# Optimization experiments

Measured on AMD Instinct MI355X. Metric: run time of the kernel, lower is better.

Reference implementation:

```python
import jax, jax.numpy as jnp
import numpy as np

B, S, H = 2, 1024, 2880
I = 2880
E = 16
K = 4


def setup_inputs() -> dict:
    key = jax.random.key(0)
    ks = jax.random.split(key, 4)
    sc = 0.02  # init scale to keep activations in a sane range
    return {
        "x": jax.random.normal(ks[0], (B, S, H), jnp.float32),
        "gate_w": jax.random.normal(ks[1], (E, H), jnp.float32) * sc,
        "gate_b": jnp.zeros((E,), jnp.float32),
        "w_gate_up": jax.random.normal(ks[2], (E, 2 * I, H), jnp.float32) * sc,
        "b_gate_up": jnp.zeros((E, 2 * I), jnp.float32),
        "w_down": jax.random.normal(ks[3], (E, H, I), jnp.float32) * sc,
        "b_down": jnp.zeros((E, H), jnp.float32),
        "swiglu_alpha": jnp.full((E,), 1.702, jnp.float32),
        "swiglu_beta": jnp.full((E,), 1.0, jnp.float32),
        "swiglu_limit": jnp.full((E,), 7.0, jnp.float32),
    }


def reference(x, gate_w, gate_b, w_gate_up, b_gate_up, w_down, b_down,
              swiglu_alpha, swiglu_beta, swiglu_limit):
    orig_shape = x.shape
    hidden = orig_shape[-1]
    t = x.reshape(-1, hidden)  # [T, H]
    T = t.shape[0]

    # Router: gate linear -> top-k -> renormalize via softmax over selected logits
    logits = t @ gate_w.T + gate_b  # [T, E]
    top_vals, top_idx = jax.lax.top_k(logits, K)  # [T, K]
    top_w = jax.nn.softmax(top_vals, axis=-1)  # RenormalizeMoeRoutingMethod
    # Dense combine matrix [T, E]; zero for non-selected experts
    combine = jnp.zeros((T, E), t.dtype).at[jnp.arange(T)[:, None], top_idx].set(top_w)

    def expert_body(acc, params):
        wgu, bgu, wd, bd, alpha, beta, lim, cw = params
        h = t @ wgu.T + bgu  # [T, 2I] fused gate_up
        glu, lin = jnp.split(h, 2, axis=-1)  # FUSED_GATE_UP_PROJ chunk
        glu = jnp.minimum(glu, lim)  # swiglu_limit clamp (gpt-oss)
        lin = jnp.clip(lin, -lim, lim)
        act = glu * jax.nn.sigmoid(alpha * glu) * (lin + beta)  # [T, I]
        y = act @ wd.T + bd  # [T, H]
        return acc + cw[:, None] * y, None

    init = jnp.zeros((T, hidden), t.dtype)
    out, _ = jax.lax.scan(
        expert_body, init,
        (w_gate_up, b_gate_up, w_down, b_down,
         swiglu_alpha, swiglu_beta, swiglu_limit, combine.T))
    return out.reshape(orig_shape)
```

## Files before the change

### kernel.cpp

```cpp
#include <hip/hip_runtime.h>
#include <stdint.h>
#include <math.h>

#define T_TOK 2048
#define H_DIM 2880
#define I_DIM 2880
#define E_NUM 16
#define TOPK 4

#define BT 128
#define BK 64
#define NK 45
#define MT_MAX 16
#define NT1 45
#define NT2 45

typedef __bf16 bf16_t;
typedef __bf16 bf16x8 __attribute__((ext_vector_type(8)));
typedef __bf16 bf16x4 __attribute__((ext_vector_type(4)));
typedef float f32x4 __attribute__((ext_vector_type(4)));

#define WAITV(N) asm volatile("s_waitcnt vmcnt(" #N ")" ::: "memory")
#define WAITL()  asm volatile("s_waitcnt lgkmcnt(0)" ::: "memory")
#define BAR()    asm volatile("s_barrier" ::: "memory")

__device__ __forceinline__ void gload16(const bf16_t* g, bf16_t* l) {
  __builtin_amdgcn_global_load_lds(
      (__attribute__((address_space(1))) const uint32_t*)g,
      (__attribute__((address_space(3))) uint32_t*)l, 16, 0, 0);
}

__device__ __forceinline__ f32x4 mfma16(bf16x8 a, bf16x8 b, f32x4 c) {
  return __builtin_amdgcn_mfma_f32_16x16x32_bf16(a, b, c, 0, 0, 0);
}

__global__ void k_prep(const float* __restrict__ x, bf16_t* __restrict__ xbf,
                       int* __restrict__ counts) {
  if (blockIdx.x == 0 && threadIdx.x < E_NUM) counts[threadIdx.x] = 0;
  int idx = blockIdx.x * 256 + threadIdx.x;
  const int total = T_TOK * H_DIM / 8;
  if (idx < total) {
    f32x4 a = ((const f32x4*)x)[2 * idx];
    f32x4 b = ((const f32x4*)x)[2 * idx + 1];
    bf16x8 o = {(bf16_t)a[0], (bf16_t)a[1], (bf16_t)a[2], (bf16_t)a[3],
                (bf16_t)b[0], (bf16_t)b[1], (bf16_t)b[2], (bf16_t)b[3]};
    ((bf16x8*)xbf)[idx] = o;
  }
}

__global__ void k_router(const float* __restrict__ x, const float* __restrict__ gw,
                         const float* __restrict__ gb, float* __restrict__ topw,
                         int* __restrict__ counts, int* __restrict__ rowsl) {
  const int t = blockIdx.x;
  const int lane = threadIdx.x;
  const int c = lane >> 4, e = lane & 15;
  const f32x4* x4 = (const f32x4*)(x + (size_t)t * H_DIM);
  const f32x4* w4 = (const f32x4*)(gw + (size_t)e * H_DIM);
  float p = 0.f;
  const int per = (H_DIM / 4) / 4;
  for (int i = c * per; i < (c + 1) * per; ++i) {
    f32x4 xv = x4[i], wv = w4[i];
    p += xv[0] * wv[0] + xv[1] * wv[1] + xv[2] * wv[2] + xv[3] * wv[3];
  }
  p += __shfl_xor(p, 16);
  p += __shfl_xor(p, 32);
  p += gb[e];
  __shared__ float lg[E_NUM];
  if (lane < E_NUM) lg[lane] = p;
  __syncthreads();
  if (lane == 0) {
    float v[E_NUM];
    #pragma unroll
    for (int i = 0; i < E_NUM; ++i) v[i] = lg[i];
    int idxs[TOPK]; float vals[TOPK];
    for (int k = 0; k < TOPK; ++k) {
      int bi = 0; float bv = -1e30f;
      for (int i = 0; i < E_NUM; ++i) {
        if (v[i] > bv) { bv = v[i]; bi = i; }
      }
      idxs[k] = bi; vals[k] = bv; v[bi] = -1e30f;
    }
    float m = vals[0], s = 0.f, w[TOPK];
    for (int k = 0; k < TOPK; ++k) { w[k] = expf(vals[k] - m); s += w[k]; }
    for (int k = 0; k < TOPK; ++k) {
      int slot = t * TOPK + k;
      topw[slot] = w[k] / s;
      int pos = atomicAdd(&counts[idxs[k]], 1);
      rowsl[idxs[k] * T_TOK + pos] = slot;
    }
  }
}


#define G1_STAGE_T(KT, BUF) do {                                        \
    int c1_ = (KT) > (NK - 1) ? (NK - 1) : (KT);                        \
    _Pragma("unroll")                                                   \
    for (int i_ = 0; i_ < 4; ++i_)                                      \
      gload16(tsrc[i_] + c1_ * BK, &sT[BUF][w * 2048 + i_ * 512]);      \
  } while (0)

#define G1_MFMA(CUR) do {                                               \
    _Pragma("unroll")                                                   \
    for (int ks = 0; ks < 2; ++ks) {                                    \
      const int koff = ks * 32 + (lane >> 4) * 8;                       \
      bf16x8 wg_[2], wl_[2], tf[4];                                     \
      _Pragma("unroll")                                                 \
      for (int wi = 0; wi < 2; ++wi) {                                  \
        int rg = 32 * wm + 16 * wi + (lane & 15);                       \
        int swz = koff ^ ((rg & 7) << 3);                               \
        wg_[wi] = *(const bf16x8*)(&sW[CUR][rg * 64 + swz]);            \
        wl_[wi] = *(const bf16x8*)(&sW[CUR][(rg + 64) * 64 + swz]);     \
      }                                                                 \
      _Pragma("unroll")                                                 \
      for (int tj = 0; tj < 4; ++tj) {                                  \
        int rt = 64 * wt + 16 * tj + (lane & 15);                       \
        tf[tj] = *(const bf16x8*)(&sT[CUR][rt * 64 + (koff ^ ((rt & 7) << 3))]); \
      }                                                                 \
      _Pragma("unroll")                                                 \
      for (int wi = 0; wi < 2; ++wi)                                    \
        _Pragma("unroll")                                               \
        for (int tj = 0; tj < 4; ++tj) {                                \
          accg[wi][tj] = mfma16(wg_[wi], tf[tj], accg[wi][tj]);         \
          accl[wi][tj] = mfma16(wl_[wi], tf[tj], accl[wi][tj]);         \
        }                                                               \
    }                                                                   \
  } while (0)

#define G1_ITER(KK, WSET) do {                                          \
    const int cur_ = (KK) & 1;                                          \
    G1_STAGE_T((KK) + 1, cur_ ^ 1);                                     \
    _Pragma("unroll")                                                   \
    for (int p_ = 0; p_ < 8; ++p_) {                                    \
      bf16x4 b_ = {(bf16_t)WSET[p_][0], (bf16_t)WSET[p_][1],            \
                   (bf16_t)WSET[p_][2], (bf16_t)WSET[p_][3]};           \
      *(bf16x4*)(&sW[cur_ ^ 1][wo[p_]]) = b_;                           \
    }                                                                   \
    { int c3_ = (KK) + 3 > (NK - 1) ? (NK - 1) : (KK) + 3;              \
      _Pragma("unroll")                                                 \
      for (int p_ = 0; p_ < 8; ++p_)                                    \
        WSET[p_] = *(const f32x4*)(wbase + wgo[p_] + c3_ * BK); }       \
    __builtin_amdgcn_s_setprio(1);                                      \
    G1_MFMA(cur_);                                                      \
    __builtin_amdgcn_s_setprio(0);                                      \
    WAITV(8); WAITL(); BAR();                                           \
  } while (0)

__global__ __launch_bounds__(256, 2)
void k_gemm1(const bf16_t* __restrict__ xbf, const float* __restrict__ wgu,
             const float* __restrict__ bgu, const float* __restrict__ al,
             const float* __restrict__ be, const float* __restrict__ lim_,
             const int* __restrict__ counts, const int* __restrict__ rowsl,
             bf16_t* __restrict__ act) {
  const int nwg = E_NUM * NT1 * MT_MAX;
  const int L = (blockIdx.x & 7) * (nwg >> 3) + (blockIdx.x >> 3);
  const int mt = L & (MT_MAX - 1);
  const int t2 = L >> 4;
  const int nt = t2 % NT1;
  const int e  = t2 / NT1;
  const int Ne = counts[e];
  const int m0 = mt * BT;
  if (m0 >= Ne) return;
  const int n0 = nt * 64;

  __shared__ alignas(16) bf16_t sW[2][128 * 64];
  __shared__ alignas(16) bf16_t sT[2][128 * 64];

  const int tid = threadIdx.x;
  const int w = tid >> 6, lane = tid & 63;
  const int wm = w & 1, wt = w >> 1;
  const int* rl = rowsl + e * T_TOK;

  const bf16_t* tsrc[4];
  {
    const int r_ = lane >> 3, cc = lane & 7;
    #pragma unroll
    for (int i = 0; i < 4; ++i) {
      int r = w * 32 + i * 8 + r_;
      int li = m0 + r; if (li > Ne - 1) li = Ne - 1;
      int tok = rl[li] >> 2;
      tsrc[i] = xbf + (size_t)tok * H_DIM + ((cc ^ (r & 7)) << 3);
    }
  }

  const int wrow = tid >> 4, wf = tid & 15;
  const float* wbase = wgu + (size_t)e * (2 * I_DIM) * H_DIM + wf * 4;
  int wgo[8], wo[8];
  #pragma unroll
  for (int p = 0; p < 8; ++p) {
    int row = wrow + p * 16;
    int grow = (row < 64) ? (n0 + row) : (I_DIM + n0 + row - 64);
    wgo[p] = grow * H_DIM;
    wo[p] = row * 64 + ((wf * 4) ^ ((row & 7) << 3));
  }

  f32x4 zero = {0.f, 0.f, 0.f, 0.f};
  f32x4 accg[2][4], accl[2][4];
  #pragma unroll
  for (int i = 0; i < 2; ++i)
    #pragma unroll
    for (int j = 0; j < 4; ++j) { accg[i][j] = zero; accl[i][j] = zero; }

  f32x4 wA[8], wB[8];
  #pragma unroll
  for (int p = 0; p < 8; ++p) wA[p] = *(const f32x4*)(wbase + wgo[p]);
  WAITV(0);
  #pragma unroll
  for (int p = 0; p < 8; ++p) {
    bf16x4 b = {(bf16_t)wA[p][0], (bf16_t)wA[p][1],
                (bf16_t)wA[p][2], (bf16_t)wA[p][3]};
    *(bf16x4*)(&sW[0][wo[p]]) = b;
  }
  G1_STAGE_T(0, 0);
  #pragma unroll
  for (int p = 0; p < 8; ++p) wA[p] = *(const f32x4*)(wbase + wgo[p] + 1 * BK);
  #pragma unroll
  for (int p = 0; p < 8; ++p) wB[p] = *(const f32x4*)(wbase + wgo[p] + 2 * BK);
  WAITV(8);
  WAITL(); BAR();

  for (int kb = 0; kb < NK - 1; kb += 2) {
    G1_ITER(kb, wA);
    G1_ITER(kb + 1, wB);
  }
  G1_ITER(NK - 1, wA);

  const float alpha = al[e], beta = be[e], lim = lim_[e];
  const float* bgp = bgu + (size_t)e * (2 * I_DIM);
  #pragma unroll
  for (int wi = 0; wi < 2; ++wi) {
    const int nb = n0 + 32 * wm + 16 * wi + ((lane >> 4) << 2);
    f32x4 bg4 = *(const f32x4*)(bgp + nb);
    f32x4 bl4 = *(const f32x4*)(bgp + I_DIM + nb);
    #pragma unroll
    for (int tj = 0; tj < 4; ++tj) {
      const int li2 = m0 + 64 * wt + 16 * tj + (lane & 15);
      if (li2 < Ne) {
        const int slot = rl[li2];
        bf16x4 ov;
        #pragma unroll
        for (int r = 0; r < 4; ++r) {
          float g = accg[wi][tj][r] + bg4[r];
          float l = accl[wi][tj][r] + bl4[r];
          g = fminf(g, lim);
          l = fminf(fmaxf(l, -lim), lim);
          float sg = 1.0f / (1.0f + expf(-alpha * g));
          ov[r] = (bf16_t)(g * sg * (l + beta));
        }
        *(bf16x4*)(&act[(size_t)slot * I_DIM + nb]) = ov;
      }
    }
  }
}


#define G2_STAGE_T(KT, BUF) do {                                        \
    int c1_ = (KT) > (NK - 1) ? (NK - 1) : (KT);                        \
    _Pragma("unroll")                                                   \
    for (int i_ = 0; i_ < 4; ++i_)                                      \
      gload16(tsrc[i_] + c1_ * BK, &sT[BUF][w * 2048 + i_ * 512]);      \
  } while (0)

#define G2_MFMA(CUR) do {                                               \
    _Pragma("unroll")                                                   \
    for (int ks = 0; ks < 2; ++ks) {                                    \
      const int koff = ks * 32 + (lane >> 4) * 8;                       \
      bf16x8 wf_[2], tf[4];                                             \
      _Pragma("unroll")                                                 \
      for (int wi = 0; wi < 2; ++wi) {                                  \
        int rg = 32 * wm + 16 * wi + (lane & 15);                       \
        wf_[wi] = *(const bf16x8*)(&sW[CUR][rg * 64 + (koff ^ ((rg & 7) << 3))]); \
      }                                                                 \
      _Pragma("unroll")                                                 \
      for (int tj = 0; tj < 4; ++tj) {                                  \
        int rt = 64 * wt + 16 * tj + (lane & 15);                       \
        tf[tj] = *(const bf16x8*)(&sT[CUR][rt * 64 + (koff ^ ((rt & 7) << 3))]); \
      }                                                                 \
      _Pragma("unroll")                                                 \
      for (int wi = 0; wi < 2; ++wi)                                    \
        _Pragma("unroll")                                               \
        for (int tj = 0; tj < 4; ++tj)                                  \
          acc[wi][tj] = mfma16(wf_[wi], tf[tj], acc[wi][tj]);           \
    }                                                                   \
  } while (0)

#define G2_ITER(KK, WSET) do {                                          \
    const int cur_ = (KK) & 1;                                          \
    G2_STAGE_T((KK) + 1, cur_ ^ 1);                                     \
    _Pragma("unroll")                                                   \
    for (int p_ = 0; p_ < 4; ++p_) {                                    \
      bf16x4 b_ = {(bf16_t)WSET[p_][0], (bf16_t)WSET[p_][1],            \
                   (bf16_t)WSET[p_][2], (bf16_t)WSET[p_][3]};           \
      *(bf16x4*)(&sW[cur_ ^ 1][wo[p_]]) = b_;                           \
    }                                                                   \
    { int c3_ = (KK) + 3 > (NK - 1) ? (NK - 1) : (KK) + 3;              \
      _Pragma("unroll")                                                 \
      for (int p_ = 0; p_ < 4; ++p_)                                    \
        WSET[p_] = *(const f32x4*)(wbase + wgo[p_] + c3_ * BK); }       \
    __builtin_amdgcn_s_setprio(1);                                      \
    G2_MFMA(cur_);                                                      \
    __builtin_amdgcn_s_setprio(0);                                      \
    WAITV(4); WAITL(); BAR();                                           \
  } while (0)

__global__ __launch_bounds__(256, 3)
void k_gemm2(const bf16_t* __restrict__ act, const float* __restrict__ wd,
             const float* __restrict__ bd, const float* __restrict__ topw,
             const int* __restrict__ counts, const int* __restrict__ rowsl,
             float* __restrict__ ybuf) {
  const int nwg = E_NUM * NT2 * MT_MAX;
  const int L = (blockIdx.x & 7) * (nwg >> 3) + (blockIdx.x >> 3);
  const int mt = L & (MT_MAX - 1);
  const int t2 = L >> 4;
  const int ht = t2 % NT2;
  const int e  = t2 / NT2;
  const int Ne = counts[e];
  const int m0 = mt * BT;
  if (m0 >= Ne) return;
  const int h0 = ht * 64;

  __shared__ alignas(16) bf16_t sW[2][64 * 64];
  __shared__ alignas(16) bf16_t sT[2][128 * 64];

  const int tid = threadIdx.x;
  const int w = tid >> 6, lane = tid & 63;
  const int wm = w & 1, wt = w >> 1;
  const int* rl = rowsl + e * T_TOK;

  const bf16_t* tsrc[4];
  {
    const int r_ = lane >> 3, cc = lane & 7;
    #pragma unroll
    for (int i = 0; i < 4; ++i) {
      int r = w * 32 + i * 8 + r_;
      int li = m0 + r; if (li > Ne - 1) li = Ne - 1;
      int slot = rl[li];
      tsrc[i] = act + (size_t)slot * I_DIM + ((cc ^ (r & 7)) << 3);
    }
  }

  const int wrow = tid >> 4, wf = tid & 15;
  const float* wbase = wd + (size_t)e * H_DIM * I_DIM + wf * 4;
  int wgo[4], wo[4];
  #pragma unroll
  for (int p = 0; p < 4; ++p) {
    int row = wrow + p * 16;
    wgo[p] = (h0 + row) * I_DIM;
    wo[p] = row * 64 + ((wf * 4) ^ ((row & 7) << 3));
  }

  f32x4 zero = {0.f, 0.f, 0.f, 0.f};
  f32x4 acc[2][4];
  #pragma unroll
  for (int i = 0; i < 2; ++i)
    #pragma unroll
    for (int j = 0; j < 4; ++j) acc[i][j] = zero;

  f32x4 wA[4], wB[4];
  #pragma unroll
  for (int p = 0; p < 4; ++p) wA[p] = *(const f32x4*)(wbase + wgo[p]);
  WAITV(0);
  #pragma unroll
  for (int p = 0; p < 4; ++p) {
    bf16x4 b = {(bf16_t)wA[p][0], (bf16_t)wA[p][1],
                (bf16_t)wA[p][2], (bf16_t)wA[p][3]};
    *(bf16x4*)(&sW[0][wo[p]]) = b;
  }
  G2_STAGE_T(0, 0);
  #pragma unroll
  for (int p = 0; p < 4; ++p) wA[p] = *(const f32x4*)(wbase + wgo[p] + 1 * BK);
  #pragma unroll
  for (int p = 0; p < 4; ++p) wB[p] = *(const f32x4*)(wbase + wgo[p] + 2 * BK);
  WAITV(4);
  WAITL(); BAR();

  for (int kb = 0; kb < NK - 1; kb += 2) {
    G2_ITER(kb, wA);
    G2_ITER(kb + 1, wB);
  }
  G2_ITER(NK - 1, wA);

  const float* bdp = bd + (size_t)e * H_DIM;
  #pragma unroll
  for (int wi = 0; wi < 2; ++wi) {
    const int hb = h0 + 32 * wm + 16 * wi + ((lane >> 4) << 2);
    f32x4 b4 = *(const f32x4*)(bdp + hb);
    #pragma unroll
    for (int tj = 0; tj < 4; ++tj) {
      const int li2 = m0 + 64 * wt + 16 * tj + (lane & 15);
      if (li2 < Ne) {
        const int slot = rl[li2];
        const float tw = topw[slot];
        f32x4 o = (acc[wi][tj] + b4) * tw;
        *(f32x4*)(&ybuf[(size_t)slot * H_DIM + hb]) = o;
      }
    }
  }
}

__global__ void k_combine(const float* __restrict__ ybuf, float* __restrict__ out) {
  const int j4 = H_DIM / 4;
  int idx = blockIdx.x * 256 + threadIdx.x;
  if (idx >= T_TOK * j4) return;
  int t = idx / j4, j = idx - t * j4;
  const f32x4* yb = (const f32x4*)ybuf;
  f32x4 s = yb[(size_t)(t * 4 + 0) * j4 + j];
  s = s + yb[(size_t)(t * 4 + 1) * j4 + j];
  s = s + yb[(size_t)(t * 4 + 2) * j4 + j];
  s = s + yb[(size_t)(t * 4 + 3) * j4 + j];
  ((f32x4*)out)[idx] = s;
}

extern "C" void kernel_launch(void* const* d_in, const int* in_sizes, int n_in,
                              void* d_out, int out_size, void* d_ws, size_t ws_size,
                              hipStream_t stream) {
  const float* x   = (const float*)d_in[0];
  const float* gw  = (const float*)d_in[1];
  const float* gb  = (const float*)d_in[2];
  const float* wgu = (const float*)d_in[3];
  const float* bgu = (const float*)d_in[4];
  const float* wd  = (const float*)d_in[5];
  const float* bd  = (const float*)d_in[6];
  const float* sal = (const float*)d_in[7];
  const float* sbe = (const float*)d_in[8];
  const float* sli = (const float*)d_in[9];
  float* out = (float*)d_out;

  char* ws = (char*)d_ws;
  int*    counts = (int*)(ws + 0);
  int*    rowsl  = (int*)(ws + 4096);
  float*  topw   = (float*)(ws + 4096 + 131072);
  bf16_t* xbf    = (bf16_t*)(ws + (1 << 20));
  bf16_t* act    = (bf16_t*)(ws + (size_t)(16 << 20));
  float*  ybuf   = (float*)(ws + (size_t)(64 << 20));

  k_prep<<<dim3(2880), dim3(256), 0, stream>>>(x, xbf, counts);
  k_router<<<dim3(T_TOK), dim3(64), 0, stream>>>(x, gw, gb, topw, counts, rowsl);
  k_gemm1<<<dim3(E_NUM * NT1 * MT_MAX), dim3(256), 0, stream>>>(
      xbf, wgu, bgu, sal, sbe, sli, counts, rowsl, act);
  k_gemm2<<<dim3(E_NUM * NT2 * MT_MAX), dim3(256), 0, stream>>>(
      act, wd, bd, topw, counts, rowsl, ybuf);
  k_combine<<<dim3(5760), dim3(256), 0, stream>>>(ybuf, out);
}
```

Before: 1.403 ms.

## Double token tile to 256 with 512-thread blocks in both expert GEMMs

Raises the token tile per workgroup from 128 to 256 and runs both expert GEMMs with 8 waves (512 threads) instead of 4. Each fp32 weight tile is then loaded and converted to bf16 once per 256 routed tokens rather than once per 128, halving repeated weight fetch and conversion work per expert. The per-thread weight staging share shrinks to match, and LDS for the token tile doubles. In exchange there are half as many workgroups, so partially filled tiles waste more work when an expert has few tokens, and register and LDS pressure per CU changes under the new launch bounds.

```diff
diff --git a/kernel.cpp b/kernel.cpp
--- a/kernel.cpp
+++ b/kernel.cpp
@@ -8,10 +8,10 @@
 #define E_NUM 16
 #define TOPK 4
 
-#define BT 128
+#define BT 256
 #define BK 64
 #define NK 45
-#define MT_MAX 16
+#define MT_MAX 8
 #define NT1 45
 #define NT2 45
 
@@ -92,11 +92,11 @@
 }
 
 
-#define G1_STAGE_T(KT, BUF) do {                                        \
+#define G_STAGE_T(KT, BUF) do {                                         \
     int c1_ = (KT) > (NK - 1) ? (NK - 1) : (KT);                        \
     _Pragma("unroll")                                                   \
     for (int i_ = 0; i_ < 4; ++i_)                                      \
-      gload16(tsrc[i_] + c1_ * BK, &sT[BUF][w * 2048 + i_ * 512]);      \
+      gload16(tsrc[i_] + c1_ * BK, &sT[BUF][wv * 2048 + i_ * 512]);     \
   } while (0)
 
 #define G1_MFMA(CUR) do {                                               \
@@ -128,24 +128,24 @@
 
 #define G1_ITER(KK, WSET) do {                                          \
     const int cur_ = (KK) & 1;                                          \
-    G1_STAGE_T((KK) + 1, cur_ ^ 1);                                     \
+    G_STAGE_T((KK) + 1, cur_ ^ 1);                                      \
     _Pragma("unroll")                                                   \
-    for (int p_ = 0; p_ < 8; ++p_) {                                    \
+    for (int p_ = 0; p_ < 4; ++p_) {                                    \
       bf16x4 b_ = {(bf16_t)WSET[p_][0], (bf16_t)WSET[p_][1],            \
                    (bf16_t)WSET[p_][2], (bf16_t)WSET[p_][3]};           \
       *(bf16x4*)(&sW[cur_ ^ 1][wo[p_]]) = b_;                           \
     }                                                                   \
     { int c3_ = (KK) + 3 > (NK - 1) ? (NK - 1) : (KK) + 3;              \
       _Pragma("unroll")                                                 \
-      for (int p_ = 0; p_ < 8; ++p_)                                    \
+      for (int p_ = 0; p_ < 4; ++p_)                                    \
         WSET[p_] = *(const f32x4*)(wbase + wgo[p_] + c3_ * BK); }       \
     __builtin_amdgcn_s_setprio(1);                                      \
     G1_MFMA(cur_);                                                      \
     __builtin_amdgcn_s_setprio(0);                                      \
-    WAITV(8); WAITL(); BAR();                                           \
+    WAITV(4); WAITL(); BAR();                                           \
   } while (0)
 
-__global__ __launch_bounds__(256, 2)
+__global__ __launch_bounds__(512, 2)
 void k_gemm1(const bf16_t* __restrict__ xbf, const float* __restrict__ wgu,
              const float* __restrict__ bgu, const float* __restrict__ al,
              const float* __restrict__ be, const float* __restrict__ lim_,
@@ -154,7 +154,7 @@
   const int nwg = E_NUM * NT1 * MT_MAX;
   const int L = (blockIdx.x & 7) * (nwg >> 3) + (blockIdx.x >> 3);
   const int mt = L & (MT_MAX - 1);
-  const int t2 = L >> 4;
+  const int t2 = L >> 3;
   const int nt = t2 % NT1;
   const int e  = t2 / NT1;
   const int Ne = counts[e];
@@ -163,11 +163,11 @@
   const int n0 = nt * 64;
 
   __shared__ alignas(16) bf16_t sW[2][128 * 64];
-  __shared__ alignas(16) bf16_t sT[2][128 * 64];
+  __shared__ alignas(16) bf16_t sT[2][256 * 64];
 
   const int tid = threadIdx.x;
-  const int w = tid >> 6, lane = tid & 63;
-  const int wm = w & 1, wt = w >> 1;
+  const int wv = tid >> 6, lane = tid & 63;
+  const int wm = wv & 1, wt = wv >> 1;
   const int* rl = rowsl + e * T_TOK;
 
   const bf16_t* tsrc[4];
@@ -175,19 +175,19 @@
     const int r_ = lane >> 3, cc = lane & 7;
     #pragma unroll
     for (int i = 0; i < 4; ++i) {
-      int r = w * 32 + i * 8 + r_;
+      int r = wv * 32 + i * 8 + r_;
       int li = m0 + r; if (li > Ne - 1) li = Ne - 1;
       int tok = rl[li] >> 2;
-      tsrc[i] = xbf + (size_t)tok * H_DIM + ((cc ^ (r & 7)) << 3);
+      tsrc[i] = xbf + (size_t)tok * H_DIM + ((cc ^ (r_ & 7)) << 3);
     }
   }
 
   const int wrow = tid >> 4, wf = tid & 15;
   const float* wbase = wgu + (size_t)e * (2 * I_DIM) * H_DIM + wf * 4;
-  int wgo[8], wo[8];
-  #pragma unroll
-  for (int p = 0; p < 8; ++p) {
-    int row = wrow + p * 16;
+  int wgo[4], wo[4];
+  #pragma unroll
+  for (int p = 0; p < 4; ++p) {
+    int row = wrow + p * 32;
     int grow = (row < 64) ? (n0 + row) : (I_DIM + n0 + row - 64);
     wgo[p] = grow * H_DIM;
     wo[p] = row * 64 + ((wf * 4) ^ ((row & 7) << 3));
@@ -200,22 +200,22 @@
     #pragma unroll
     for (int j = 0; j < 4; ++j) { accg[i][j] = zero; accl[i][j] = zero; }
 
-  f32x4 wA[8], wB[8];
-  #pragma unroll
-  for (int p = 0; p < 8; ++p) wA[p] = *(const f32x4*)(wbase + wgo[p]);
+  f32x4 wA[4], wB[4];
+  #pragma unroll
+  for (int p = 0; p < 4; ++p) wA[p] = *(const f32x4*)(wbase + wgo[p]);
   WAITV(0);
   #pragma unroll
-  for (int p = 0; p < 8; ++p) {
+  for (int p = 0; p < 4; ++p) {
     bf16x4 b = {(bf16_t)wA[p][0], (bf16_t)wA[p][1],
                 (bf16_t)wA[p][2], (bf16_t)wA[p][3]};
     *(bf16x4*)(&sW[0][wo[p]]) = b;
   }
-  G1_STAGE_T(0, 0);
-  #pragma unroll
-  for (int p = 0; p < 8; ++p) wA[p] = *(const f32x4*)(wbase + wgo[p] + 1 * BK);
-  #pragma unroll
-  for (int p = 0; p < 8; ++p) wB[p] = *(const f32x4*)(wbase + wgo[p] + 2 * BK);
-  WAITV(8);
+  G_STAGE_T(0, 0);
+  #pragma unroll
+  for (int p = 0; p < 4; ++p) wA[p] = *(const f32x4*)(wbase + wgo[p] + 1 * BK);
+  #pragma unroll
+  for (int p = 0; p < 4; ++p) wB[p] = *(const f32x4*)(wbase + wgo[p] + 2 * BK);
+  WAITV(4);
   WAITL(); BAR();
 
   for (int kb = 0; kb < NK - 1; kb += 2) {
@@ -253,13 +253,6 @@
 }
 
 
-#define G2_STAGE_T(KT, BUF) do {                                        \
-    int c1_ = (KT) > (NK - 1) ? (NK - 1) : (KT);                        \
-    _Pragma("unroll")                                                   \
-    for (int i_ = 0; i_ < 4; ++i_)                                      \
-      gload16(tsrc[i_] + c1_ * BK, &sT[BUF][w * 2048 + i_ * 512]);      \
-  } while (0)
-
 #define G2_MFMA(CUR) do {                                               \
     _Pragma("unroll")                                                   \
     for (int ks = 0; ks < 2; ++ks) {                                    \
@@ -285,24 +278,24 @@
 
 #define G2_ITER(KK, WSET) do {                                          \
     const int cur_ = (KK) & 1;                                          \
-    G2_STAGE_T((KK) + 1, cur_ ^ 1);                                     \
+    G_STAGE_T((KK) + 1, cur_ ^ 1);                                      \
     _Pragma("unroll")                                                   \
-    for (int p_ = 0; p_ < 4; ++p_) {                                    \
+    for (int p_ = 0; p_ < 2; ++p_) {                                    \
       bf16x4 b_ = {(bf16_t)WSET[p_][0], (bf16_t)WSET[p_][1],            \
                    (bf16_t)WSET[p_][2], (bf16_t)WSET[p_][3]};           \
       *(bf16x4*)(&sW[cur_ ^ 1][wo[p_]]) = b_;                           \
     }                                                                   \
     { int c3_ = (KK) + 3 > (NK - 1) ? (NK - 1) : (KK) + 3;              \
       _Pragma("unroll")                                                 \
-      for (int p_ = 0; p_ < 4; ++p_)                                    \
+      for (int p_ = 0; p_ < 2; ++p_)                                    \
         WSET[p_] = *(const f32x4*)(wbase + wgo[p_] + c3_ * BK); }       \
     __builtin_amdgcn_s_setprio(1);                                      \
     G2_MFMA(cur_);                                                      \
     __builtin_amdgcn_s_setprio(0);                                      \
-    WAITV(4); WAITL(); BAR();                                           \
+    WAITV(2); WAITL(); BAR();                                           \
   } while (0)
 
-__global__ __launch_bounds__(256, 3)
+__global__ __launch_bounds__(512, 4)
 void k_gemm2(const bf16_t* __restrict__ act, const float* __restrict__ wd,
              const float* __restrict__ bd, const float* __restrict__ topw,
              const int* __restrict__ counts, const int* __restrict__ rowsl,
@@ -310,7 +303,7 @@
   const int nwg = E_NUM * NT2 * MT_MAX;
   const int L = (blockIdx.x & 7) * (nwg >> 3) + (blockIdx.x >> 3);
   const int mt = L & (MT_MAX - 1);
-  const int t2 = L >> 4;
+  const int t2 = L >> 3;
   const int ht = t2 % NT2;
   const int e  = t2 / NT2;
   const int Ne = counts[e];
@@ -319,11 +312,11 @@
   const int h0 = ht * 64;
 
   __shared__ alignas(16) bf16_t sW[2][64 * 64];
-  __shared__ alignas(16) bf16_t sT[2][128 * 64];
+  __shared__ alignas(16) bf16_t sT[2][256 * 64];
 
   const int tid = threadIdx.x;
-  const int w = tid >> 6, lane = tid & 63;
-  const int wm = w & 1, wt = w >> 1;
+  const int wv = tid >> 6, lane = tid & 63;
+  const int wm = wv & 1, wt = wv >> 1;
   const int* rl = rowsl + e * T_TOK;
 
   const bf16_t* tsrc[4];
@@ -331,19 +324,19 @@
     const int r_ = lane >> 3, cc = lane & 7;
     #pragma unroll
     for (int i = 0; i < 4; ++i) {
-      int r = w * 32 + i * 8 + r_;
+      int r = wv * 32 + i * 8 + r_;
       int li = m0 + r; if (li > Ne - 1) li = Ne - 1;
       int slot = rl[li];
-      tsrc[i] = act + (size_t)slot * I_DIM + ((cc ^ (r & 7)) << 3);
+      tsrc[i] = act + (size_t)slot * I_DIM + ((cc ^ (r_ & 7)) << 3);
     }
   }
 
   const int wrow = tid >> 4, wf = tid & 15;
   const float* wbase = wd + (size_t)e * H_DIM * I_DIM + wf * 4;
-  int wgo[4], wo[4];
-  #pragma unroll
-  for (int p = 0; p < 4; ++p) {
-    int row = wrow + p * 16;
+  int wgo[2], wo[2];
+  #pragma unroll
+  for (int p = 0; p < 2; ++p) {
+    int row = wrow + p * 32;
     wgo[p] = (h0 + row) * I_DIM;
     wo[p] = row * 64 + ((wf * 4) ^ ((row & 7) << 3));
   }
@@ -355,22 +348,22 @@
     #pragma unroll
     for (int j = 0; j < 4; ++j) acc[i][j] = zero;
 
-  f32x4 wA[4], wB[4];
-  #pragma unroll
-  for (int p = 0; p < 4; ++p) wA[p] = *(const f32x4*)(wbase + wgo[p]);
+  f32x4 wA[2], wB[2];
+  #pragma unroll
+  for (int p = 0; p < 2; ++p) wA[p] = *(const f32x4*)(wbase + wgo[p]);
   WAITV(0);
   #pragma unroll
-  for (int p = 0; p < 4; ++p) {
+  for (int p = 0; p < 2; ++p) {
     bf16x4 b = {(bf16_t)wA[p][0], (bf16_t)wA[p][1],
                 (bf16_t)wA[p][2], (bf16_t)wA[p][3]};
     *(bf16x4*)(&sW[0][wo[p]]) = b;
   }
-  G2_STAGE_T(0, 0);
-  #pragma unroll
-  for (int p = 0; p < 4; ++p) wA[p] = *(const f32x4*)(wbase + wgo[p] + 1 * BK);
-  #pragma unroll
-  for (int p = 0; p < 4; ++p) wB[p] = *(const f32x4*)(wbase + wgo[p] + 2 * BK);
-  WAITV(4);
+  G_STAGE_T(0, 0);
+  #pragma unroll
+  for (int p = 0; p < 2; ++p) wA[p] = *(const f32x4*)(wbase + wgo[p] + 1 * BK);
+  #pragma unroll
+  for (int p = 0; p < 2; ++p) wB[p] = *(const f32x4*)(wbase + wgo[p] + 2 * BK);
+  WAITV(2);
   WAITL(); BAR();
 
   for (int kb = 0; kb < NK - 1; kb += 2) {
@@ -435,9 +428,9 @@
 
   k_prep<<<dim3(2880), dim3(256), 0, stream>>>(x, xbf, counts);
   k_router<<<dim3(T_TOK), dim3(64), 0, stream>>>(x, gw, gb, topw, counts, rowsl);
-  k_gemm1<<<dim3(E_NUM * NT1 * MT_MAX), dim3(256), 0, stream>>>(
+  k_gemm1<<<dim3(E_NUM * NT1 * MT_MAX), dim3(512), 0, stream>>>(
       xbf, wgu, bgu, sal, sbe, sli, counts, rowsl, act);
-  k_gemm2<<<dim3(E_NUM * NT2 * MT_MAX), dim3(256), 0, stream>>>(
+  k_gemm2<<<dim3(E_NUM * NT2 * MT_MAX), dim3(512), 0, stream>>>(
       act, wd, bd, topw, counts, rowsl, ybuf);
   k_combine<<<dim3(5760), dim3(256), 0, stream>>>(ybuf, out);
 }
```

Measured after the change: 1.546 ms. 1.1x slower.
